# Kernel optimization log

Hardware: AMD Instinct MI355X
Metric: run time of the kernel (lower is better)

Reference implementation:

```python
import jax, jax.numpy as jnp
import numpy as np

EPS = 1e-8

def _cosine_rows(a, b):
    na = jnp.maximum(jnp.linalg.norm(a, axis=1), EPS)
    nb = jnp.maximum(jnp.linalg.norm(b, axis=1), EPS)
    return jnp.sum(a * b, axis=1) / (na * nb)


def setup_inputs() -> dict:
    key = jax.random.key(0)
    k1, k2 = jax.random.split(key)
    X = jax.random.normal(k1, (16384, 1024), dtype=jnp.float32)
    dictionary = jax.random.normal(k2, (4096, 1024), dtype=jnp.float32)
    descriptors = jnp.arange(4096, dtype=jnp.int64)
    return {"X": X, "dictionary": dictionary, "descriptors": descriptors, "k": 16}


def reference(X, dictionary, descriptors, k):
    # SOMP with centering=True, criterion='l1', pc=None (default forward path)
    orig_X = X
    std_orig_sum = jnp.sum(jnp.var(orig_X, axis=0, ddof=1))
    X_mean = jnp.mean(X, axis=0, keepdims=True)   # [1, D]
    Xc = X - X_mean                               # centered data [N, D]

    M = dictionary.shape[0]
    notchosen = jnp.ones((M,), dtype=X.dtype)
    residual = Xc
    chosen, evr, l2, cosine = [], [], [], []
    W = None
    recon = jnp.zeros_like(Xc)

    for i in range(k):  # k is a static Python int -> unrolled, per-step shapes static
        cross = residual @ dictionary.T           # [N, M] -- dominant memory traffic
        scores = jnp.sum(jnp.abs(cross * notchosen), axis=0)  # l1 criterion
        idx = jnp.argmax(scores)
        chosen.append(idx)
        notchosen = notchosen.at[idx].set(0)

        atoms = dictionary[jnp.stack(chosen)]     # [i+1, D], dynamic gather, static shape
        # least squares: min ||atoms.T @ W - Xc.T||  (full column rank -> normal eqs)
        G = atoms @ atoms.T                       # [i+1, i+1]
        W = jnp.linalg.solve(G, atoms @ Xc.T)     # [i+1, N]
        recon = (atoms.T @ W).T                   # [N, D]
        residual = Xc - recon

        rec_full = X_mean + recon
        evr.append(jnp.sum(jnp.var(rec_full, axis=0, ddof=1)) / std_orig_sum)
        cosine.append(jnp.mean(_cosine_rows(orig_X, rec_full)))
        l2.append(jnp.mean((orig_X - rec_full) ** 2))

    weights = jnp.linalg.norm(W, axis=1)          # [k]
    chosen_arr = jnp.stack(chosen)
    recon_out = X_mean + recon
    residual_out = Xc - recon                     # == X - recon_out
    return (recon_out, residual_out, chosen_arr, weights, W.T,
            jnp.stack(evr), jnp.stack(l2), jnp.stack(cosine))
```

## Files before the change

kernel.cpp:

```cpp
#include <hip/hip_runtime.h>
#include <math.h>

#define NROWS 16384
#define DIMK  1024
#define MDIC  4096
#define KSEL  16

#define OFF_RECON   0
#define OFF_RESID   ((size_t)NROWS*DIMK)
#define OFF_CHOSEN  ((size_t)2*NROWS*DIMK)
#define OFF_WEIGHTS (OFF_CHOSEN + 16)
#define OFF_WT      (OFF_WEIGHTS + 16)
#define OFF_EVR     (OFF_WT + (size_t)NROWS*KSEL)
#define OFF_L2      (OFF_EVR + 16)
#define OFF_COS     (OFF_L2 + 16)

typedef unsigned short u16;
typedef unsigned long long u64;
typedef __attribute__((ext_vector_type(8))) short short8;
typedef __attribute__((ext_vector_type(4))) float f32x4;

__device__ inline float blockReduce256f(float v) {
    __shared__ float ws_[4];
    #pragma unroll
    for (int off = 32; off > 0; off >>= 1) v += __shfl_down(v, off);
    __syncthreads();
    if ((threadIdx.x & 63) == 0) ws_[threadIdx.x >> 6] = v;
    __syncthreads();
    return ws_[0] + ws_[1] + ws_[2] + ws_[3];
}

__device__ inline double blockReduceD(double v) {
    __shared__ double sred[4];
    #pragma unroll
    for (int off = 32; off > 0; off >>= 1) v += __shfl_down(v, off);
    __syncthreads();
    if ((threadIdx.x & 63) == 0) sred[threadIdx.x >> 6] = v;
    __syncthreads();
    return sred[0] + sred[1] + sred[2] + sred[3];
}

__device__ inline u16 f2bf(float f) {
    unsigned u = __float_as_uint(f);
    unsigned r = u + 0x7FFFu + ((u >> 16) & 1u);
    return (u16)(r >> 16);
}
__device__ inline float bf2f(u16 h) { return __uint_as_float(((unsigned)h) << 16); }

__global__ void k_init(float* notchosen, u64* amx) {
    int m = blockIdx.x * 256 + threadIdx.x;
    if (m < MDIC) notchosen[m] = 1.0f;
    if (blockIdx.x == 0 && threadIdx.x < 2) amx[threadIdx.x] = 0ULL;
}

__global__ __launch_bounds__(256) void k_colstats(const float* __restrict__ X,
                                                  float* __restrict__ colpart,
                                                  float* __restrict__ sqpart) {
    int d  = blockIdx.x * 256 + threadIdx.x;
    int r0 = blockIdx.y * 256;
    float s = 0.f, sq = 0.f;
    for (int r = 0; r < 256; ++r) {
        float v = X[(size_t)(r0 + r) * DIMK + d];
        s += v; sq += v * v;
    }
    colpart[(size_t)blockIdx.y * DIMK + d] = s;
    __shared__ float red[256];
    red[threadIdx.x] = sq; __syncthreads();
    for (int off = 128; off > 0; off >>= 1) {
        if (threadIdx.x < off) red[threadIdx.x] += red[threadIdx.x + off];
        __syncthreads();
    }
    if (threadIdx.x == 0) sqpart[blockIdx.y * 4 + blockIdx.x] = red[0];
}

__global__ __launch_bounds__(1024) void k_reduce_mean(const float* __restrict__ colpart,
                                                      const float* __restrict__ sqpart,
                                                      float* __restrict__ xmean,
                                                      double* __restrict__ scal) {
    int d = threadIdx.x;
    double s = 0.0;
    for (int y = 0; y < 64; ++y) s += (double)colpart[(size_t)y * DIMK + d];
    float m = (float)(s / (double)NROWS);
    xmean[d] = m;
    __shared__ double red[1024];
    red[d] = (double)m * (double)m; __syncthreads();
    for (int off = 512; off > 0; off >>= 1) {
        if (d < off) red[d] += red[d + off];
        __syncthreads();
    }
    if (d == 0) {
        double xmn2 = red[0];
        double sx2 = 0.0;
        for (int i = 0; i < 256; ++i) sx2 += (double)sqpart[i];
        scal[0] = sx2;
        scal[1] = sx2 - (double)NROWS * xmn2;
        scal[2] = xmn2;
    }
}

__global__ __launch_bounds__(256) void k_md(const float* __restrict__ Dict,
                                            const float* __restrict__ xmean,
                                            float* __restrict__ md) {
    int m = blockIdx.x, t = threadIdx.x;
    float4 a = ((const float4*)(Dict + (size_t)m * DIMK))[t];
    float4 b = ((const float4*)xmean)[t];
    float s = a.x * b.x + a.y * b.y + a.z * b.z + a.w * b.w;
    s = blockReduce256f(s);
    if (t == 0) md[m] = s;
}

__global__ __launch_bounds__(256) void k_rowstats(const float* __restrict__ X,
                                                  const float* __restrict__ xmean,
                                                  float* __restrict__ Xnorm2,
                                                  float* __restrict__ XdotM) {
    int n = blockIdx.x, t = threadIdx.x;
    float4 x = ((const float4*)(X + (size_t)n * DIMK))[t];
    float4 m = ((const float4*)xmean)[t];
    float s2 = x.x * x.x + x.y * x.y + x.z * x.z + x.w * x.w;
    float sm = x.x * m.x + x.y * m.y + x.z * m.z + x.w * m.w;
    s2 = blockReduce256f(s2);
    sm = blockReduce256f(sm);
    if (t == 0) { Xnorm2[n] = s2; XdotM[n] = sm; }
}

__global__ __launch_bounds__(256) void k_split(const float* __restrict__ src,
                                               u16* __restrict__ hi,
                                               u16* __restrict__ lo) {
    size_t idx = ((size_t)blockIdx.x * 256 + threadIdx.x) * 4;
    float4 v = *(const float4*)(src + idx);
    ushort4 h, l;
    h.x = f2bf(v.x); l.x = f2bf(v.x - bf2f(h.x));
    h.y = f2bf(v.y); l.y = f2bf(v.y - bf2f(h.y));
    h.z = f2bf(v.z); l.z = f2bf(v.z - bf2f(h.z));
    h.w = f2bf(v.w); l.w = f2bf(v.w - bf2f(h.w));
    *(ushort4*)(hi + idx) = h;
    *(ushort4*)(lo + idx) = l;
}

__global__ __launch_bounds__(256) void k_gemm_mfma(const u16* __restrict__ Ahi,
                                                   const u16* __restrict__ Alo,
                                                   const u16* __restrict__ Bhi,
                                                   const u16* __restrict__ Blo,
                                                   const float* __restrict__ md,
                                                   u16* __restrict__ C0h,
                                                   int rowAbase) {
    __shared__ u16 sAh[128 * 32];
    __shared__ u16 sAl[128 * 32];
    __shared__ u16 sBh[128 * 32];
    __shared__ u16 sBl[128 * 32];
    int tid  = threadIdx.x;
    int wave = tid >> 6, lane = tid & 63;
    int rowA0 = blockIdx.y * 128;
    int rowB0 = blockIdx.x * 128;

    const u16* gsrc = (wave == 0) ? Ahi : (wave == 1) ? Alo : (wave == 2) ? Bhi : Blo;
    u16* sdst       = (wave == 0) ? sAh : (wave == 1) ? sAl : (wave == 2) ? sBh : sBl;
    int grow0 = (wave < 2) ? rowA0 : rowB0;
    const u16* gbase = gsrc + (size_t)(grow0 + (lane >> 2)) * DIMK + ((lane & 3) << 3);

    f32x4 zero = {0.f, 0.f, 0.f, 0.f};
    f32x4 acc[4][4];
    #pragma unroll
    for (int i = 0; i < 4; ++i)
        #pragma unroll
        for (int j = 0; j < 4; ++j) acc[i][j] = zero;

    int lm = lane & 15, lk = lane >> 4;
    int wi = wave >> 1, wj = wave & 1;

    for (int k0 = 0; k0 < DIMK; k0 += 32) {
        __syncthreads();
        #pragma unroll
        for (int i = 0; i < 8; ++i) {
            __builtin_amdgcn_global_load_lds(
                (__attribute__((address_space(1))) void*)(gbase + k0 + (size_t)i * 16 * DIMK),
                (__attribute__((address_space(3))) void*)(sdst + i * 512),
                16, 0, 0);
        }
        __syncthreads();
        short8 ah[4], al[4], bh[4], bl[4];
        #pragma unroll
        for (int f = 0; f < 4; ++f) {
            int ra = (wi * 64 + f * 16 + lm) * 32 + lk * 8;
            ah[f] = *(const short8*)&sAh[ra];
            al[f] = *(const short8*)&sAl[ra];
            int rb = (wj * 64 + f * 16 + lm) * 32 + lk * 8;
            bh[f] = *(const short8*)&sBh[rb];
            bl[f] = *(const short8*)&sBl[rb];
        }
        #pragma unroll
        for (int fi = 0; fi < 4; ++fi)
            #pragma unroll
            for (int fj = 0; fj < 4; ++fj) {
                acc[fi][fj] = __builtin_amdgcn_mfma_f32_16x16x32_bf16(ah[fi], bh[fj], acc[fi][fj], 0, 0, 0);
                acc[fi][fj] = __builtin_amdgcn_mfma_f32_16x16x32_bf16(ah[fi], bl[fj], acc[fi][fj], 0, 0, 0);
                acc[fi][fj] = __builtin_amdgcn_mfma_f32_16x16x32_bf16(al[fi], bh[fj], acc[fi][fj], 0, 0, 0);
            }
    }
    #pragma unroll
    for (int fj = 0; fj < 4; ++fj) {
        int m = rowB0 + wj * 64 + fj * 16 + lm;
        float mdv = md[m];
        #pragma unroll
        for (int fi = 0; fi < 4; ++fi) {
            int nb = rowAbase + rowA0 + wi * 64 + fi * 16 + lk * 4;
            #pragma unroll
            for (int r = 0; r < 4; ++r)
                C0h[(size_t)(nb + r) * MDIC + m] = f2bf(acc[fi][fj][r] - mdv);
        }
    }
}

template <int NA>
__global__ __launch_bounds__(256) void k_score(const u16* __restrict__ C0h,
                                               const float* __restrict__ GR,
                                               const float* __restrict__ Wm,
                                               float* __restrict__ scorePf) {
    constexpr int NAX = NA ? NA : 1;
    __shared__ float Wl[NAX][64];
    int t = threadIdx.x;
    int m0 = blockIdx.x * 1024 + t * 4;
    int n0 = blockIdx.y * 64;
    float4 gr[NAX];
    #pragma unroll
    for (int j = 0; j < NA; ++j) gr[j] = *(const float4*)&GR[(size_t)j * MDIC + m0];
    for (int idx = t; idx < NA * 64; idx += 256) {
        int j = idx >> 6, nn = idx & 63;
        Wl[j][nn] = Wm[(size_t)j * NROWS + n0 + nn];
    }
    __syncthreads();
    float4 acc = {0.f, 0.f, 0.f, 0.f};
    for (int nn = 0; nn < 64; ++nn) {
        ushort4 ch = *(const ushort4*)&C0h[(size_t)(n0 + nn) * MDIC + m0];
        float4 c = {bf2f(ch.x), bf2f(ch.y), bf2f(ch.z), bf2f(ch.w)};
        float4 cr = {0.f, 0.f, 0.f, 0.f};
        #pragma unroll
        for (int j = 0; j < NA; ++j) {
            float wv = Wl[j][nn];
            cr.x += wv * gr[j].x; cr.y += wv * gr[j].y;
            cr.z += wv * gr[j].z; cr.w += wv * gr[j].w;
        }
        acc.x += fabsf(c.x - cr.x); acc.y += fabsf(c.y - cr.y);
        acc.z += fabsf(c.z - cr.z); acc.w += fabsf(c.w - cr.w);
    }
    *(float4*)&scorePf[(size_t)blockIdx.y * MDIC + m0] = acc;
}

__global__ __launch_bounds__(256) void k_scoreargmax(const float* __restrict__ scorePf,
                                                     float* __restrict__ notchosen,
                                                     u64* __restrict__ amx,
                                                     int* __restrict__ chosen,
                                                     float* __restrict__ outChosen,
                                                     int iter) {
    int t = threadIdx.x;
    int m = blockIdx.x * 256 + t;
    double s = 0.0;
    for (int y = 0; y < 256; ++y) s += (double)scorePf[(size_t)y * MDIC + m];
    u64 key = 0ULL;
    if (notchosen[m] != 0.f) {
        u64 bits = (u64)__double_as_longlong(s);
        key = (bits & ~0xFFFULL) | (u64)(4095 - m);
    }
    __shared__ u64 sk[256];
    sk[t] = key; __syncthreads();
    for (int off = 128; off > 0; off >>= 1) {
        if (t < off) { if (sk[t + off] > sk[t]) sk[t] = sk[t + off]; }
        __syncthreads();
    }
    if (t == 0) {
        atomicMax(&amx[0], sk[0]);
        __threadfence();
        u64 done = atomicAdd(&amx[1], 1ULL);
        if (done == 15ULL) {
            u64 k = atomicMax(&amx[0], 0ULL);
            int c = 4095 - (int)(k & 0xFFFULL);
            chosen[iter] = c;
            notchosen[c] = 0.f;
            outChosen[iter] = (float)c;
            amx[0] = 0ULL; amx[1] = 0ULL;
            __threadfence();
        }
    }
}

__global__ __launch_bounds__(256) void k_gramgather(const float* __restrict__ Dict,
                                                    const int* __restrict__ chosen,
                                                    const u16* __restrict__ C0h,
                                                    float* __restrict__ GR,
                                                    float* __restrict__ Bm, int iter) {
    int t = threadIdx.x;
    int c = chosen[iter];
    if (blockIdx.x < MDIC) {
        int m = blockIdx.x;
        float4 a = ((const float4*)(Dict + (size_t)c * DIMK))[t];
        float4 b = ((const float4*)(Dict + (size_t)m * DIMK))[t];
        float s = a.x * b.x + a.y * b.y + a.z * b.z + a.w * b.w;
        s = blockReduce256f(s);
        if (t == 0) GR[(size_t)iter * MDIC + m] = s;
    } else {
        int n = (blockIdx.x - MDIC) * 256 + t;
        Bm[(size_t)iter * NROWS + n] = bf2f(C0h[(size_t)n * MDIC + c]);
    }
}

__global__ __launch_bounds__(256) void k_chol(const float* __restrict__ GR,
                                              const float* __restrict__ mdv,
                                              const int* __restrict__ chosen,
                                              float* __restrict__ Lmat,
                                              float* __restrict__ Gcc,
                                              float* __restrict__ mdot, int nat) {
    __shared__ float G[16][16];
    __shared__ float L[16][16];
    int t = threadIdx.x;
    if (t < nat * nat) {
        int a = t / nat, b = t % nat;
        G[a][b] = GR[(size_t)a * MDIC + chosen[b]];
    }
    if (t < nat) mdot[t] = mdv[chosen[t]];
    __syncthreads();
    if (t == 0) {
        for (int a = 0; a < nat; ++a)
            for (int b = 0; b <= a; ++b) {
                float s = G[a][b];
                for (int x = 0; x < b; ++x) s -= L[a][x] * L[b][x];
                L[a][b] = (a == b) ? sqrtf(fmaxf(s, 1e-20f)) : s / L[b][b];
            }
    }
    __syncthreads();
    if (t < nat * nat) {
        int a = t / nat, b = t % nat;
        Gcc[a * 16 + b]  = G[a][b];
        Lmat[a * 16 + b] = (b <= a) ? L[a][b] : 0.f;
    }
}

template <int NAT>
__global__ __launch_bounds__(256) void k_solvestats(const float* __restrict__ Bm,
                                                    const float* __restrict__ Lmat,
                                                    const float* __restrict__ Gcc,
                                                    const float* __restrict__ mdot,
                                                    const float* __restrict__ Xnorm2,
                                                    const float* __restrict__ XdotM,
                                                    const double* __restrict__ scal,
                                                    float* __restrict__ Wm,
                                                    double* __restrict__ statsP) {
    __shared__ float L[16][16];
    __shared__ float G[16][16];
    __shared__ float mdl[16];
    int t = threadIdx.x;
    if (t < NAT * NAT) {
        L[t / NAT][t % NAT] = Lmat[(t / NAT) * 16 + (t % NAT)];
        G[t / NAT][t % NAT] = Gcc[(t / NAT) * 16 + (t % NAT)];
    }
    if (t < NAT) mdl[t] = mdot[t];
    __syncthreads();
    int n = blockIdx.x * 256 + t;
    float b[NAT], y[NAT], w[NAT];
    #pragma unroll
    for (int j = 0; j < NAT; ++j) b[j] = Bm[(size_t)j * NROWS + n];
    #pragma unroll
    for (int a = 0; a < NAT; ++a) {
        float s = b[a];
        #pragma unroll
        for (int x = 0; x < NAT; ++x) if (x < a) s -= L[a][x] * y[x];
        y[a] = s / L[a][a];
    }
    #pragma unroll
    for (int a = NAT - 1; a >= 0; --a) {
        float s = y[a];
        #pragma unroll
        for (int x = 0; x < NAT; ++x) if (x > a) s -= L[x][a] * w[x];
        w[a] = s / L[a][a];
    }
    #pragma unroll
    for (int j = 0; j < NAT; ++j) Wm[(size_t)j * NROWS + n] = w[j];

    float q = 0.f, wb = 0.f, wmd = 0.f, num1 = 0.f;
    #pragma unroll
    for (int j = 0; j < NAT; ++j) {
        float gw = 0.f;
        #pragma unroll
        for (int x = 0; x < NAT; ++x) gw += G[j][x] * w[x];
        q    += w[j] * gw;
        wb   += w[j] * b[j];
        wmd  += w[j] * mdl[j];
        num1 += w[j] * (b[j] + mdl[j]);
    }
    float xmn2 = (float)scal[2];
    float rec2 = xmn2 + 2.f * wmd + q;
    float na = fmaxf(sqrtf(Xnorm2[n]), 1e-8f);
    float nb = fmaxf(sqrtf(fmaxf(rec2, 0.f)), 1e-8f);
    float cosn = (XdotM[n] + num1) / (na * nb);

    double r0 = blockReduceD((double)q);
    double r1 = blockReduceD((double)wb);
    double r2 = blockReduceD((double)cosn);
    if (t == 0) {
        statsP[(size_t)blockIdx.x * 40 + 0] = r0;
        statsP[(size_t)blockIdx.x * 40 + 1] = r1;
        statsP[(size_t)blockIdx.x * 40 + 2] = r2;
    }
    for (int j = 0; j < NAT; ++j) {
        double rw = blockReduceD((double)w[j]);
        double rq = blockReduceD((double)w[j] * (double)w[j]);
        if (t == 0) {
            statsP[(size_t)blockIdx.x * 40 + 3 + j]  = rw;
            statsP[(size_t)blockIdx.x * 40 + 19 + j] = rq;
        }
    }
}

template <int NAT>
__global__ __launch_bounds__(64) void k_finalize(const double* __restrict__ statsP,
                                                 const float* __restrict__ Gcc,
                                                 const double* __restrict__ scal,
                                                 float* __restrict__ out, int iter) {
    int t = threadIdx.x;
    double q  = statsP[(size_t)t * 40 + 0];
    double wb = statsP[(size_t)t * 40 + 1];
    double cs = statsP[(size_t)t * 40 + 2];
    double ws[NAT], wq[NAT];
    #pragma unroll
    for (int j = 0; j < NAT; ++j) {
        ws[j] = statsP[(size_t)t * 40 + 3 + j];
        wq[j] = statsP[(size_t)t * 40 + 19 + j];
    }
    #pragma unroll
    for (int off = 32; off > 0; off >>= 1) {
        q  += __shfl_down(q, off);
        wb += __shfl_down(wb, off);
        cs += __shfl_down(cs, off);
        #pragma unroll
        for (int j = 0; j < NAT; ++j) {
            ws[j] += __shfl_down(ws[j], off);
            wq[j] += __shfl_down(wq[j], off);
        }
    }
    double wbar[NAT];
    #pragma unroll
    for (int j = 0; j < NAT; ++j) wbar[j] = __shfl(ws[j], 0) / (double)NROWS;
    double wg = 0.0;
    for (int idx = t; idx < NAT * NAT; idx += 64) {
        int a = idx / NAT, b = idx % NAT;
        wg += wbar[a] * wbar[b] * (double)Gcc[a * 16 + b];
    }
    #pragma unroll
    for (int off = 32; off > 0; off >>= 1) wg += __shfl_down(wg, off);
    if (t == 0) {
        double sumXc2 = scal[1];
        out[OFF_EVR + iter] = (float)((q - (double)NROWS * wg) / sumXc2);
        out[OFF_L2  + iter] = (float)((sumXc2 - 2.0 * wb + q) / ((double)NROWS * (double)DIMK));
        out[OFF_COS + iter] = (float)(cs / (double)NROWS);
        if (NAT == KSEL) {
            for (int j = 0; j < NAT; ++j)
                out[OFF_WEIGHTS + j] = (float)sqrt(wq[j]);
        }
    }
}

__global__ __launch_bounds__(256) void k_outfinal(const float* __restrict__ X,
                                                  const float* __restrict__ xmean,
                                                  const float* __restrict__ Dict,
                                                  const int* __restrict__ chosen,
                                                  const float* __restrict__ Wm,
                                                  float* __restrict__ out) {
    __shared__ int cI[16];
    int t = threadIdx.x;
    if (t < 16) cI[t] = chosen[t];
    __syncthreads();
    int n0 = blockIdx.x * 8;
    float4 xm = ((const float4*)xmean)[t];
    for (int r = 0; r < 8; ++r) {
        int n = n0 + r;
        float w[16];
        #pragma unroll
        for (int j = 0; j < 16; ++j) w[j] = Wm[(size_t)j * NROWS + n];
        float4 rec = xm;
        #pragma unroll
        for (int j = 0; j < 16; ++j) {
            float4 a = ((const float4*)(Dict + (size_t)cI[j] * DIMK))[t];
            rec.x += w[j] * a.x; rec.y += w[j] * a.y;
            rec.z += w[j] * a.z; rec.w += w[j] * a.w;
        }
        float4 xv = ((const float4*)(X + (size_t)n * DIMK))[t];
        float4 res = {xv.x - rec.x, xv.y - rec.y, xv.z - rec.z, xv.w - rec.w};
        ((float4*)(out + OFF_RECON + (size_t)n * DIMK))[t] = rec;
        ((float4*)(out + OFF_RESID + (size_t)n * DIMK))[t] = res;
    }
}

__global__ __launch_bounds__(256) void k_wt(const float* __restrict__ Wm,
                                            float* __restrict__ out) {
    int idx = blockIdx.x * 256 + threadIdx.x;
    int n = idx >> 4, j = idx & 15;
    out[OFF_WT + idx] = Wm[(size_t)j * NROWS + n];
}

struct IterArgs {
    const float *X, *Dict;
    u16 *C0h;
    float *GR, *W, *Bm, *md, *xmean, *Xnorm2, *XdotM, *notchosen, *Lmat, *Gcc, *mdot;
    float *scorePf;
    u64 *amx;
    double *scal, *statsP;
    int *chosen;
    float *out;
    hipStream_t stream;
};

template <int I>
static void run_iter(const IterArgs& a) {
    k_score<I><<<dim3(4, 256), 256, 0, a.stream>>>(a.C0h, a.GR, a.W, a.scorePf);
    k_scoreargmax<<<16, 256, 0, a.stream>>>(a.scorePf, a.notchosen, a.amx, a.chosen,
                                            a.out + OFF_CHOSEN, I);
    k_gramgather<<<MDIC + 64, 256, 0, a.stream>>>(a.Dict, a.chosen, a.C0h, a.GR, a.Bm, I);
    k_chol<<<1, 256, 0, a.stream>>>(a.GR, a.md, a.chosen, a.Lmat, a.Gcc, a.mdot, I + 1);
    k_solvestats<I + 1><<<64, 256, 0, a.stream>>>(a.Bm, a.Lmat, a.Gcc, a.mdot,
                                                  a.Xnorm2, a.XdotM, a.scal, a.W, a.statsP);
    k_finalize<I + 1><<<1, 64, 0, a.stream>>>(a.statsP, a.Gcc, a.scal, a.out, I);
}

template <int I>
struct Loop {
    static void go(const IterArgs& a) { run_iter<I>(a); Loop<I + 1>::go(a); }
};
template <>
struct Loop<KSEL> { static void go(const IterArgs&) {} };

extern "C" void kernel_launch(void* const* d_in, const int* in_sizes, int n_in,
                              void* d_out, int out_size, void* d_ws, size_t ws_size,
                              hipStream_t stream) {
    (void)in_sizes; (void)n_in; (void)out_size;
    const float* X    = (const float*)d_in[0];
    const float* Dict = (const float*)d_in[1];
    float* out = (float*)d_out;

    char* ws = (char*)d_ws;
    size_t off = 0;
    auto carve = [&](size_t bytes) -> char* {
        char* p = ws + off;
        off += (bytes + 255) & ~(size_t)255;
        return p;
    };
    u16*    C0h       = (u16*)   carve((size_t)NROWS * MDIC * 2);
    float*  GR        = (float*) carve((size_t)KSEL * MDIC * 4);
    float*  W         = (float*) carve((size_t)KSEL * NROWS * 4);
    float*  Bm        = (float*) carve((size_t)KSEL * NROWS * 4);
    float*  md        = (float*) carve((size_t)MDIC * 4);
    float*  xmean     = (float*) carve((size_t)DIMK * 4);
    float*  colpart   = (float*) carve((size_t)64 * DIMK * 4);
    float*  sqpart    = (float*) carve(256 * 4);
    float*  Xnorm2    = (float*) carve((size_t)NROWS * 4);
    float*  XdotM     = (float*) carve((size_t)NROWS * 4);
    float*  scorePf   = (float*) carve((size_t)256 * MDIC * 4);
    float*  notchosen = (float*) carve((size_t)MDIC * 4);
    u64*    amx       = (u64*)   carve(2 * 8);
    int*    chosen    = (int*)   carve(KSEL * 4);
    float*  Lmat      = (float*) carve(256 * 4);
    float*  Gcc       = (float*) carve(256 * 4);
    float*  mdot      = (float*) carve(16 * 4);
    double* scal      = (double*)carve(8 * 8);
    double* statsP    = (double*)carve((size_t)64 * 40 * 8);
    u16*    Bhi       = (u16*)   carve((size_t)MDIC * DIMK * 2);
    u16*    Blo       = (u16*)   carve((size_t)MDIC * DIMK * 2);

    int chunkrows = 0;
    for (int cr = NROWS; cr >= 128; cr >>= 1) {
        size_t need = (size_t)cr * DIMK * 2 * 2 + 512;
        if (off + need <= ws_size) { chunkrows = cr; break; }
    }
    if (chunkrows == 0) chunkrows = 128;
    u16* Ahi = (u16*) carve((size_t)chunkrows * DIMK * 2);
    u16* Alo = (u16*) carve((size_t)chunkrows * DIMK * 2);

    k_init<<<MDIC / 256, 256, 0, stream>>>(notchosen, amx);
    k_colstats<<<dim3(4, 64), 256, 0, stream>>>(X, colpart, sqpart);
    k_reduce_mean<<<1, 1024, 0, stream>>>(colpart, sqpart, xmean, scal);
    k_md<<<MDIC, 256, 0, stream>>>(Dict, xmean, md);
    k_rowstats<<<NROWS, 256, 0, stream>>>(X, xmean, Xnorm2, XdotM);

    k_split<<<(MDIC * DIMK) / 1024, 256, 0, stream>>>(Dict, Bhi, Blo);
    int nchunks = NROWS / chunkrows;
    for (int c = 0; c < nchunks; ++c) {
        k_split<<<(chunkrows * DIMK) / 1024, 256, 0, stream>>>(
            X + (size_t)c * chunkrows * DIMK, Ahi, Alo);
        k_gemm_mfma<<<dim3(MDIC / 128, chunkrows / 128), 256, 0, stream>>>(
            Ahi, Alo, Bhi, Blo, md, C0h, c * chunkrows);
    }

    IterArgs a{X, Dict, C0h, GR, W, Bm, md, xmean, Xnorm2, XdotM, notchosen,
               Lmat, Gcc, mdot, scorePf, amx, scal, statsP, chosen, out, stream};
    Loop<0>::go(a);

    k_outfinal<<<NROWS / 8, 256, 0, stream>>>(X, xmean, Dict, chosen, W, out);
    k_wt<<<NROWS * KSEL / 256, 256, 0, stream>>>(W, out);
}
```

Measured before the change: 1.802 ms.

## Fuse per-iteration SOMP kernels and make the Cholesky update incremental

Merges the per-iteration chain of argmax, gram gather, Cholesky, solve-stats and finalize kernels into two kernels. The last argmax block now extends the Cholesky factor by one row using a precomputed dictionary norm. The solve kernel runs alongside the gram row computation, gathers its own B column, and finishes the stats with fixed-point atomics and a last-block counter. It also fuses the row stats into the X split kernel and the W transpose into the output kernel, cutting launch count and extra passes over X. The cost is fixed-point rounding of the statistics and more reliance on atomic last-block patterns.

```diff
diff --git a/kernel.cpp b/kernel.cpp
--- a/kernel.cpp
+++ b/kernel.cpp
@@ -30,14 +30,10 @@
     return ws_[0] + ws_[1] + ws_[2] + ws_[3];
 }
 
-__device__ inline double blockReduceD(double v) {
-    __shared__ double sred[4];
+__device__ inline void wredStore(double v, int k, int lane, int wv, double (*accS)[4]) {
     #pragma unroll
     for (int off = 32; off > 0; off >>= 1) v += __shfl_down(v, off);
-    __syncthreads();
-    if ((threadIdx.x & 63) == 0) sred[threadIdx.x >> 6] = v;
-    __syncthreads();
-    return sred[0] + sred[1] + sred[2] + sred[3];
+    if (lane == 0) accS[k][wv] = v;
 }
 
 __device__ inline u16 f2bf(float f) {
@@ -47,10 +43,14 @@
 }
 __device__ inline float bf2f(u16 h) { return __uint_as_float(((unsigned)h) << 16); }
 
-__global__ void k_init(float* notchosen, u64* amx) {
+__global__ void k_init(float* notchosen, u64* amx, u64* statsAcc, u64* ctr2) {
     int m = blockIdx.x * 256 + threadIdx.x;
     if (m < MDIC) notchosen[m] = 1.0f;
-    if (blockIdx.x == 0 && threadIdx.x < 2) amx[threadIdx.x] = 0ULL;
+    if (blockIdx.x == 0) {
+        if (threadIdx.x < 40) statsAcc[threadIdx.x] = 0ULL;
+        if (threadIdx.x < 2)  amx[threadIdx.x] = 0ULL;
+        if (threadIdx.x == 0) *ctr2 = 0ULL;
+    }
 }
 
 __global__ __launch_bounds__(256) void k_colstats(const float* __restrict__ X,
@@ -100,27 +100,16 @@
 
 __global__ __launch_bounds__(256) void k_md(const float* __restrict__ Dict,
                                             const float* __restrict__ xmean,
-                                            float* __restrict__ md) {
+                                            float* __restrict__ md,
+                                            float* __restrict__ Dnorm2) {
     int m = blockIdx.x, t = threadIdx.x;
     float4 a = ((const float4*)(Dict + (size_t)m * DIMK))[t];
     float4 b = ((const float4*)xmean)[t];
-    float s = a.x * b.x + a.y * b.y + a.z * b.z + a.w * b.w;
-    s = blockReduce256f(s);
-    if (t == 0) md[m] = s;
-}
-
-__global__ __launch_bounds__(256) void k_rowstats(const float* __restrict__ X,
-                                                  const float* __restrict__ xmean,
-                                                  float* __restrict__ Xnorm2,
-                                                  float* __restrict__ XdotM) {
-    int n = blockIdx.x, t = threadIdx.x;
-    float4 x = ((const float4*)(X + (size_t)n * DIMK))[t];
-    float4 m = ((const float4*)xmean)[t];
-    float s2 = x.x * x.x + x.y * x.y + x.z * x.z + x.w * x.w;
-    float sm = x.x * m.x + x.y * m.y + x.z * m.z + x.w * m.w;
-    s2 = blockReduce256f(s2);
-    sm = blockReduce256f(sm);
-    if (t == 0) { Xnorm2[n] = s2; XdotM[n] = sm; }
+    float s  = a.x * b.x + a.y * b.y + a.z * b.z + a.w * b.w;
+    float sn = a.x * a.x + a.y * a.y + a.z * a.z + a.w * a.w;
+    s  = blockReduce256f(s);
+    sn = blockReduce256f(sn);
+    if (t == 0) { md[m] = s; Dnorm2[m] = sn; }
 }
 
 __global__ __launch_bounds__(256) void k_split(const float* __restrict__ src,
@@ -135,6 +124,30 @@
     h.w = f2bf(v.w); l.w = f2bf(v.w - bf2f(h.w));
     *(ushort4*)(hi + idx) = h;
     *(ushort4*)(lo + idx) = l;
+}
+
+__global__ __launch_bounds__(256) void k_splitX(const float* __restrict__ src,
+                                                u16* __restrict__ hi,
+                                                u16* __restrict__ lo,
+                                                const float* __restrict__ xmean,
+                                                float* __restrict__ Xnorm2,
+                                                float* __restrict__ XdotM) {
+    int n = blockIdx.x, t = threadIdx.x;
+    size_t idx = (size_t)n * DIMK + t * 4;
+    float4 v = *(const float4*)(src + idx);
+    float4 mv = ((const float4*)xmean)[t];
+    ushort4 h, l;
+    h.x = f2bf(v.x); l.x = f2bf(v.x - bf2f(h.x));
+    h.y = f2bf(v.y); l.y = f2bf(v.y - bf2f(h.y));
+    h.z = f2bf(v.z); l.z = f2bf(v.z - bf2f(h.z));
+    h.w = f2bf(v.w); l.w = f2bf(v.w - bf2f(h.w));
+    *(ushort4*)(hi + idx) = h;
+    *(ushort4*)(lo + idx) = l;
+    float s2 = v.x * v.x + v.y * v.y + v.z * v.z + v.w * v.w;
+    float sm = v.x * mv.x + v.y * mv.y + v.z * mv.z + v.w * mv.w;
+    s2 = blockReduce256f(s2);
+    sm = blockReduce256f(sm);
+    if (t == 0) { Xnorm2[n] = s2; XdotM[n] = sm; }
 }
 
 __global__ __launch_bounds__(256) void k_gemm_mfma(const u16* __restrict__ Ahi,
@@ -251,113 +264,136 @@
                                                      u64* __restrict__ amx,
                                                      int* __restrict__ chosen,
                                                      float* __restrict__ outChosen,
+                                                     const float* __restrict__ md,
+                                                     const float* __restrict__ Dnorm2,
+                                                     const float* __restrict__ GR,
+                                                     float* __restrict__ Lmat,
+                                                     float* __restrict__ Gcc,
+                                                     float* __restrict__ mdot,
                                                      int iter) {
     int t = threadIdx.x;
-    int m = blockIdx.x * 256 + t;
-    double s = 0.0;
-    for (int y = 0; y < 256; ++y) s += (double)scorePf[(size_t)y * MDIC + m];
-    u64 key = 0ULL;
-    if (notchosen[m] != 0.f) {
-        u64 bits = (u64)__double_as_longlong(s);
-        key = (bits & ~0xFFFULL) | (u64)(4095 - m);
-    }
-    __shared__ u64 sk[256];
-    sk[t] = key; __syncthreads();
-    for (int off = 128; off > 0; off >>= 1) {
-        if (t < off) { if (sk[t + off] > sk[t]) sk[t] = sk[t + off]; }
-        __syncthreads();
-    }
+    int m0 = blockIdx.x * 256;
+    int tm = t & 63, yg = t >> 6;
+    float sx = 0.f, sy = 0.f, sz = 0.f, sw = 0.f;
+    #pragma unroll 4
+    for (int y = yg; y < 256; y += 4) {
+        float4 v = *(const float4*)&scorePf[(size_t)y * MDIC + m0 + (tm << 2)];
+        sx += v.x; sy += v.y; sz += v.z; sw += v.w;
+    }
+    __shared__ float4 red4[4][64];
+    float4 pv; pv.x = sx; pv.y = sy; pv.z = sz; pv.w = sw;
+    red4[yg][tm] = pv;
+    __syncthreads();
+    u64 best = 0ULL;
+    if (t < 64) {
+        float4 a = red4[0][t], b = red4[1][t], cc = red4[2][t], d = red4[3][t];
+        double sv[4] = {(double)a.x + b.x + cc.x + d.x,
+                        (double)a.y + b.y + cc.y + d.y,
+                        (double)a.z + b.z + cc.z + d.z,
+                        (double)a.w + b.w + cc.w + d.w};
+        int mb = m0 + (t << 2);
+        #pragma unroll
+        for (int j = 0; j < 4; ++j) {
+            if (notchosen[mb + j] != 0.f) {
+                u64 key = ((u64)__double_as_longlong(sv[j]) & ~0xFFFULL) | (u64)(4095 - (mb + j));
+                if (key > best) best = key;
+            }
+        }
+        #pragma unroll
+        for (int off = 32; off > 0; off >>= 1) {
+            u64 o = __shfl_down(best, off);
+            if (o > best) best = o;
+        }
+    }
+    __shared__ int slast, sc;
     if (t == 0) {
-        atomicMax(&amx[0], sk[0]);
+        atomicMax(&amx[0], best);
         __threadfence();
         u64 done = atomicAdd(&amx[1], 1ULL);
-        if (done == 15ULL) {
+        slast = (done == 15ULL) ? 1 : 0;
+        if (slast) {
             u64 k = atomicMax(&amx[0], 0ULL);
             int c = 4095 - (int)(k & 0xFFFULL);
+            sc = c;
             chosen[iter] = c;
             notchosen[c] = 0.f;
             outChosen[iter] = (float)c;
+            mdot[iter] = md[c];
             amx[0] = 0ULL; amx[1] = 0ULL;
-            __threadfence();
-        }
-    }
-}
-
-__global__ __launch_bounds__(256) void k_gramgather(const float* __restrict__ Dict,
-                                                    const int* __restrict__ chosen,
-                                                    const u16* __restrict__ C0h,
-                                                    float* __restrict__ GR,
-                                                    float* __restrict__ Bm, int iter) {
+        }
+    }
+    __syncthreads();
+    if (!slast) return;
+    int c = sc;
+    __shared__ float Lsh[16][16];
+    __shared__ float g[17];
+    __shared__ float LrowS[16];
+    Lsh[t >> 4][t & 15] = Lmat[t];
+    if (t < iter)  g[t] = GR[(size_t)t * MDIC + c];
+    if (t == iter) g[t] = Dnorm2[c];
+    __syncthreads();
+    if (t == 0) {
+        for (int b = 0; b < iter; ++b) {
+            float s = g[b];
+            for (int x = 0; x < b; ++x) s -= LrowS[x] * Lsh[b][x];
+            LrowS[b] = s / Lsh[b][b];
+        }
+        float s2 = g[iter];
+        for (int x = 0; x < iter; ++x) s2 -= LrowS[x] * LrowS[x];
+        LrowS[iter] = sqrtf(fmaxf(s2, 1e-20f));
+        for (int b = 0; b <= iter; ++b) Lmat[iter * 16 + b] = LrowS[b];
+        for (int b = iter + 1; b < 16; ++b) Lmat[iter * 16 + b] = 0.f;
+        for (int b = 0; b < iter; ++b) { Gcc[iter * 16 + b] = g[b]; Gcc[b * 16 + iter] = g[b]; }
+        Gcc[iter * 16 + iter] = g[iter];
+    }
+}
+
+template <int NAT>
+__global__ __launch_bounds__(256) void k_gramsolve(const float* __restrict__ Dict,
+                                                   const int* __restrict__ chosen,
+                                                   const u16* __restrict__ C0h,
+                                                   float* __restrict__ GR,
+                                                   float* __restrict__ Bm,
+                                                   const float* __restrict__ Lmat,
+                                                   const float* __restrict__ Gcc_g,
+                                                   const float* __restrict__ mdot,
+                                                   const float* __restrict__ Xnorm2,
+                                                   const float* __restrict__ XdotM,
+                                                   const double* __restrict__ scal,
+                                                   float* __restrict__ Wm,
+                                                   u64* __restrict__ statsAcc,
+                                                   u64* __restrict__ ctr2,
+                                                   float* __restrict__ out, int iter) {
     int t = threadIdx.x;
     int c = chosen[iter];
-    if (blockIdx.x < MDIC) {
-        int m = blockIdx.x;
+    if (blockIdx.x >= 64) {
+        int m = blockIdx.x - 64;
         float4 a = ((const float4*)(Dict + (size_t)c * DIMK))[t];
         float4 b = ((const float4*)(Dict + (size_t)m * DIMK))[t];
         float s = a.x * b.x + a.y * b.y + a.z * b.z + a.w * b.w;
         s = blockReduce256f(s);
         if (t == 0) GR[(size_t)iter * MDIC + m] = s;
-    } else {
-        int n = (blockIdx.x - MDIC) * 256 + t;
-        Bm[(size_t)iter * NROWS + n] = bf2f(C0h[(size_t)n * MDIC + c]);
-    }
-}
-
-__global__ __launch_bounds__(256) void k_chol(const float* __restrict__ GR,
-                                              const float* __restrict__ mdv,
-                                              const int* __restrict__ chosen,
-                                              float* __restrict__ Lmat,
-                                              float* __restrict__ Gcc,
-                                              float* __restrict__ mdot, int nat) {
-    __shared__ float G[16][16];
-    __shared__ float L[16][16];
-    int t = threadIdx.x;
-    if (t < nat * nat) {
-        int a = t / nat, b = t % nat;
-        G[a][b] = GR[(size_t)a * MDIC + chosen[b]];
-    }
-    if (t < nat) mdot[t] = mdv[chosen[t]];
-    __syncthreads();
-    if (t == 0) {
-        for (int a = 0; a < nat; ++a)
-            for (int b = 0; b <= a; ++b) {
-                float s = G[a][b];
-                for (int x = 0; x < b; ++x) s -= L[a][x] * L[b][x];
-                L[a][b] = (a == b) ? sqrtf(fmaxf(s, 1e-20f)) : s / L[b][b];
-            }
-    }
-    __syncthreads();
-    if (t < nat * nat) {
-        int a = t / nat, b = t % nat;
-        Gcc[a * 16 + b]  = G[a][b];
-        Lmat[a * 16 + b] = (b <= a) ? L[a][b] : 0.f;
-    }
-}
-
-template <int NAT>
-__global__ __launch_bounds__(256) void k_solvestats(const float* __restrict__ Bm,
-                                                    const float* __restrict__ Lmat,
-                                                    const float* __restrict__ Gcc,
-                                                    const float* __restrict__ mdot,
-                                                    const float* __restrict__ Xnorm2,
-                                                    const float* __restrict__ XdotM,
-                                                    const double* __restrict__ scal,
-                                                    float* __restrict__ Wm,
-                                                    double* __restrict__ statsP) {
+        return;
+    }
+    constexpr int NV = 3 + 2 * NAT;
     __shared__ float L[16][16];
     __shared__ float G[16][16];
     __shared__ float mdl[16];
-    int t = threadIdx.x;
+    __shared__ double accS[35][4];
     if (t < NAT * NAT) {
-        L[t / NAT][t % NAT] = Lmat[(t / NAT) * 16 + (t % NAT)];
-        G[t / NAT][t % NAT] = Gcc[(t / NAT) * 16 + (t % NAT)];
+        int a = t / NAT, b2 = t % NAT;
+        L[a][b2] = Lmat[a * 16 + b2];
+        G[a][b2] = Gcc_g[a * 16 + b2];
     }
     if (t < NAT) mdl[t] = mdot[t];
     __syncthreads();
     int n = blockIdx.x * 256 + t;
     float b[NAT], y[NAT], w[NAT];
     #pragma unroll
-    for (int j = 0; j < NAT; ++j) b[j] = Bm[(size_t)j * NROWS + n];
+    for (int j = 0; j < NAT - 1; ++j) b[j] = Bm[(size_t)j * NROWS + n];
+    float bn = bf2f(C0h[(size_t)n * MDIC + c]);
+    b[NAT - 1] = bn;
+    Bm[(size_t)(NAT - 1) * NROWS + n] = bn;
     #pragma unroll
     for (int a = 0; a < NAT; ++a) {
         float s = b[a];
@@ -392,68 +428,52 @@
     float nb = fmaxf(sqrtf(fmaxf(rec2, 0.f)), 1e-8f);
     float cosn = (XdotM[n] + num1) / (na * nb);
 
-    double r0 = blockReduceD((double)q);
-    double r1 = blockReduceD((double)wb);
-    double r2 = blockReduceD((double)cosn);
+    int lane = t & 63, wv = t >> 6;
+    wredStore((double)q,    0, lane, wv, accS);
+    wredStore((double)wb,   1, lane, wv, accS);
+    wredStore((double)cosn, 2, lane, wv, accS);
+    #pragma unroll
+    for (int j = 0; j < NAT; ++j) {
+        wredStore((double)w[j],                 3 + j,       lane, wv, accS);
+        wredStore((double)w[j] * (double)w[j],  3 + NAT + j, lane, wv, accS);
+    }
+    __syncthreads();
+    if (t < NV) {
+        double tot = accS[t][0] + accS[t][1] + accS[t][2] + accS[t][3];
+        long long fx = (long long)(tot * 1048576.0);
+        atomicAdd(&statsAcc[t], (u64)fx);
+    }
+    __shared__ int slast2;
+    __syncthreads();
     if (t == 0) {
-        statsP[(size_t)blockIdx.x * 40 + 0] = r0;
-        statsP[(size_t)blockIdx.x * 40 + 1] = r1;
-        statsP[(size_t)blockIdx.x * 40 + 2] = r2;
-    }
-    for (int j = 0; j < NAT; ++j) {
-        double rw = blockReduceD((double)w[j]);
-        double rq = blockReduceD((double)w[j] * (double)w[j]);
-        if (t == 0) {
-            statsP[(size_t)blockIdx.x * 40 + 3 + j]  = rw;
-            statsP[(size_t)blockIdx.x * 40 + 19 + j] = rq;
-        }
-    }
-}
-
-template <int NAT>
-__global__ __launch_bounds__(64) void k_finalize(const double* __restrict__ statsP,
-                                                 const float* __restrict__ Gcc,
-                                                 const double* __restrict__ scal,
-                                                 float* __restrict__ out, int iter) {
-    int t = threadIdx.x;
-    double q  = statsP[(size_t)t * 40 + 0];
-    double wb = statsP[(size_t)t * 40 + 1];
-    double cs = statsP[(size_t)t * 40 + 2];
-    double ws[NAT], wq[NAT];
-    #pragma unroll
-    for (int j = 0; j < NAT; ++j) {
-        ws[j] = statsP[(size_t)t * 40 + 3 + j];
-        wq[j] = statsP[(size_t)t * 40 + 19 + j];
-    }
-    #pragma unroll
-    for (int off = 32; off > 0; off >>= 1) {
-        q  += __shfl_down(q, off);
-        wb += __shfl_down(wb, off);
-        cs += __shfl_down(cs, off);
-        #pragma unroll
-        for (int j = 0; j < NAT; ++j) {
-            ws[j] += __shfl_down(ws[j], off);
-            wq[j] += __shfl_down(wq[j], off);
-        }
-    }
-    double wbar[NAT];
-    #pragma unroll
-    for (int j = 0; j < NAT; ++j) wbar[j] = __shfl(ws[j], 0) / (double)NROWS;
-    double wg = 0.0;
-    for (int idx = t; idx < NAT * NAT; idx += 64) {
-        int a = idx / NAT, b = idx % NAT;
-        wg += wbar[a] * wbar[b] * (double)Gcc[a * 16 + b];
-    }
-    #pragma unroll
-    for (int off = 32; off > 0; off >>= 1) wg += __shfl_down(wg, off);
+        __threadfence();
+        slast2 = (atomicAdd(ctr2, 1ULL) == 63ULL) ? 1 : 0;
+    }
+    __syncthreads();
+    if (!slast2) return;
+    __shared__ double stot[35];
+    __shared__ double wbarS[16];
+    if (t < NV) {
+        u64 raw = atomicAdd(&statsAcc[t], 0ULL);
+        stot[t] = (double)(long long)raw * (1.0 / 1048576.0);
+        statsAcc[t] = 0ULL;
+    }
+    if (t == 0) *ctr2 = 0ULL;
+    __syncthreads();
+    if (t < NAT) wbarS[t] = stot[3 + t] * (1.0 / (double)NROWS);
+    __syncthreads();
     if (t == 0) {
+        double q2 = stot[0], wb2 = stot[1], cs = stot[2];
+        double wg = 0.0;
+        for (int a = 0; a < NAT; ++a)
+            for (int b2 = 0; b2 < NAT; ++b2) wg += wbarS[a] * wbarS[b2] * (double)G[a][b2];
         double sumXc2 = scal[1];
-        out[OFF_EVR + iter] = (float)((q - (double)NROWS * wg) / sumXc2);
-        out[OFF_L2  + iter] = (float)((sumXc2 - 2.0 * wb + q) / ((double)NROWS * (double)DIMK));
+        out[OFF_EVR + iter] = (float)((q2 - (double)NROWS * wg) / sumXc2);
+        out[OFF_L2  + iter] = (float)((sumXc2 - 2.0 * wb2 + q2) / ((double)NROWS * (double)DIMK));
         out[OFF_COS + iter] = (float)(cs / (double)NROWS);
         if (NAT == KSEL) {
             for (int j = 0; j < NAT; ++j)
-                out[OFF_WEIGHTS + j] = (float)sqrt(wq[j]);
+                out[OFF_WEIGHTS + j] = (float)sqrt(stot[3 + NAT + j]);
         }
     }
 }
@@ -469,6 +489,11 @@
     if (t < 16) cI[t] = chosen[t];
     __syncthreads();
     int n0 = blockIdx.x * 8;
+    if (t < 128) {
+        int j = t & 15, r = t >> 4;
+        int n = n0 + r;
+        out[OFF_WT + (size_t)n * 16 + j] = Wm[(size_t)j * NROWS + n];
+    }
     float4 xm = ((const float4*)xmean)[t];
     for (int r = 0; r < 8; ++r) {
         int n = n0 + r;
@@ -489,20 +514,13 @@
     }
 }
 
-__global__ __launch_bounds__(256) void k_wt(const float* __restrict__ Wm,
-                                            float* __restrict__ out) {
-    int idx = blockIdx.x * 256 + threadIdx.x;
-    int n = idx >> 4, j = idx & 15;
-    out[OFF_WT + idx] = Wm[(size_t)j * NROWS + n];
-}
-
 struct IterArgs {
     const float *X, *Dict;
     u16 *C0h;
-    float *GR, *W, *Bm, *md, *xmean, *Xnorm2, *XdotM, *notchosen, *Lmat, *Gcc, *mdot;
+    float *GR, *W, *Bm, *md, *Dnorm2, *xmean, *Xnorm2, *XdotM, *notchosen, *Lmat, *Gcc, *mdot;
     float *scorePf;
-    u64 *amx;
-    double *scal, *statsP;
+    u64 *amx, *statsAcc, *ctr2;
+    double *scal;
     int *chosen;
     float *out;
     hipStream_t stream;
@@ -512,12 +530,12 @@
 static void run_iter(const IterArgs& a) {
     k_score<I><<<dim3(4, 256), 256, 0, a.stream>>>(a.C0h, a.GR, a.W, a.scorePf);
     k_scoreargmax<<<16, 256, 0, a.stream>>>(a.scorePf, a.notchosen, a.amx, a.chosen,
-                                            a.out + OFF_CHOSEN, I);
-    k_gramgather<<<MDIC + 64, 256, 0, a.stream>>>(a.Dict, a.chosen, a.C0h, a.GR, a.Bm, I);
-    k_chol<<<1, 256, 0, a.stream>>>(a.GR, a.md, a.chosen, a.Lmat, a.Gcc, a.mdot, I + 1);
-    k_solvestats<I + 1><<<64, 256, 0, a.stream>>>(a.Bm, a.Lmat, a.Gcc, a.mdot,
-                                                  a.Xnorm2, a.XdotM, a.scal, a.W, a.statsP);
-    k_finalize<I + 1><<<1, 64, 0, a.stream>>>(a.statsP, a.Gcc, a.scal, a.out, I);
+                                            a.out + OFF_CHOSEN, a.md, a.Dnorm2, a.GR,
+                                            a.Lmat, a.Gcc, a.mdot, I);
+    k_gramsolve<I + 1><<<MDIC + 64, 256, 0, a.stream>>>(a.Dict, a.chosen, a.C0h, a.GR,
+                                                        a.Bm, a.Lmat, a.Gcc, a.mdot,
+                                                        a.Xnorm2, a.XdotM, a.scal, a.W,
+                                                        a.statsAcc, a.ctr2, a.out, I);
 }
 
 template <int I>
@@ -547,6 +565,7 @@
     float*  W         = (float*) carve((size_t)KSEL * NROWS * 4);
     float*  Bm        = (float*) carve((size_t)KSEL * NROWS * 4);
     float*  md        = (float*) carve((size_t)MDIC * 4);
+    float*  Dnorm2    = (float*) carve((size_t)MDIC * 4);
     float*  xmean     = (float*) carve((size_t)DIMK * 4);
     float*  colpart   = (float*) carve((size_t)64 * DIMK * 4);
     float*  sqpart    = (float*) carve(256 * 4);
@@ -555,12 +574,13 @@
     float*  scorePf   = (float*) carve((size_t)256 * MDIC * 4);
     float*  notchosen = (float*) carve((size_t)MDIC * 4);
     u64*    amx       = (u64*)   carve(2 * 8);
+    u64*    statsAcc  = (u64*)   carve(40 * 8);
+    u64*    ctr2      = (u64*)   carve(8);
     int*    chosen    = (int*)   carve(KSEL * 4);
     float*  Lmat      = (float*) carve(256 * 4);
     float*  Gcc       = (float*) carve(256 * 4);
     float*  mdot      = (float*) carve(16 * 4);
     double* scal      = (double*)carve(8 * 8);
-    double* statsP    = (double*)carve((size_t)64 * 40 * 8);
     u16*    Bhi       = (u16*)   carve((size_t)MDIC * DIMK * 2);
     u16*    Blo       = (u16*)   carve((size_t)MDIC * DIMK * 2);
 
@@ -573,25 +593,24 @@
     u16* Ahi = (u16*) carve((size_t)chunkrows * DIMK * 2);
     u16* Alo = (u16*) carve((size_t)chunkrows * DIMK * 2);
 
-    k_init<<<MDIC / 256, 256, 0, stream>>>(notchosen, amx);
+    k_init<<<MDIC / 256, 256, 0, stream>>>(notchosen, amx, statsAcc, ctr2);
     k_colstats<<<dim3(4, 64), 256, 0, stream>>>(X, colpart, sqpart);
     k_reduce_mean<<<1, 1024, 0, stream>>>(colpart, sqpart, xmean, scal);
-    k_md<<<MDIC, 256, 0, stream>>>(Dict, xmean, md);
-    k_rowstats<<<NROWS, 256, 0, stream>>>(X, xmean, Xnorm2, XdotM);
+    k_md<<<MDIC, 256, 0, stream>>>(Dict, xmean, md, Dnorm2);
 
     k_split<<<(MDIC * DIMK) / 1024, 256, 0, stream>>>(Dict, Bhi, Blo);
     int nchunks = NROWS / chunkrows;
     for (int c = 0; c < nchunks; ++c) {
-        k_split<<<(chunkrows * DIMK) / 1024, 256, 0, stream>>>(
-            X + (size_t)c * chunkrows * DIMK, Ahi, Alo);
+        k_splitX<<<chunkrows, 256, 0, stream>>>(
+            X + (size_t)c * chunkrows * DIMK, Ahi, Alo, xmean,
+            Xnorm2 + (size_t)c * chunkrows, XdotM + (size_t)c * chunkrows);
         k_gemm_mfma<<<dim3(MDIC / 128, chunkrows / 128), 256, 0, stream>>>(
             Ahi, Alo, Bhi, Blo, md, C0h, c * chunkrows);
     }
 
-    IterArgs a{X, Dict, C0h, GR, W, Bm, md, xmean, Xnorm2, XdotM, notchosen,
-               Lmat, Gcc, mdot, scorePf, amx, scal, statsP, chosen, out, stream};
+    IterArgs a{X, Dict, C0h, GR, W, Bm, md, Dnorm2, xmean, Xnorm2, XdotM, notchosen,
+               Lmat, Gcc, mdot, scorePf, amx, statsAcc, ctr2, scal, chosen, out, stream};
     Loop<0>::go(a);
 
     k_outfinal<<<NROWS / 8, 256, 0, stream>>>(X, xmean, Dict, chosen, W, out);
-    k_wt<<<NROWS * KSEL / 256, 256, 0, stream>>>(W, out);
-}
+}
```

New measurement: 1.471 ms. 18.4% less time.
